# Optimization experiments

Hardware: AMD Instinct MI355X
Metric: run time of the kernel (lower is better)

## Reference

```python
import jax, jax.numpy as jnp
import numpy as np

B, S, D = 4, 2048, 1024
P = 2
N_FEAT = 16          # n_feature_know
N_REST = 16          # n_restore_know
R = 128              # knowledge_rank
D_SPACE = 64


def setup_inputs() -> dict:
    key = jax.random.key(0)
    ks = jax.random.split(key, 6)
    x = jax.random.normal(ks[0], (B, S, D), dtype=jnp.float32)
    # per-token routing weights for each of P feature paths, in [0,1)
    feature_paths = jax.random.uniform(ks[1], (P, B, S, N_FEAT), dtype=jnp.float32)
    f_know = jax.random.normal(ks[2], (N_FEAT, D, R), dtype=jnp.float32) * 0.02
    r_know = jax.random.normal(ks[3], (N_REST, R, D), dtype=jnp.float32) * 0.02
    feature_emb = jax.random.normal(ks[4], (N_FEAT, D_SPACE), dtype=jnp.float32)
    W_router = jax.random.normal(ks[5], (D_SPACE + R, N_REST), dtype=jnp.float32) * 0.05
    return {"x": x, "feature_paths": feature_paths, "f_know": f_know,
            "r_know": r_know, "feature_emb": feature_emb, "W_router": W_router}


def reference(x, feature_paths, f_know, r_know, feature_emb, W_router):
    # Feature projection into all N low-rank banks: [B,S,N,R]
    all_h = jnp.einsum('bsd,ndr->bsnr', x, f_know)
    # Weighted sum over banks per path: [P,B,S,R]
    h_all = jnp.einsum('bsnr,pbsn->pbsr', all_h, feature_paths)
    # Context for restore routing: [P,B,S,D_SPACE]
    neuron_ctx = jnp.einsum('pbsn,nd->pbsd', feature_paths, feature_emb)
    # restore_input = cat([neuron_ctx, h]) -> router -> softmax restore weights
    restore_input = jnp.concatenate([neuron_ctx, h_all], axis=-1)  # [P,B,S,D_SPACE+R]
    logits = jnp.einsum('pbsc,cn->pbsn', restore_input, W_router)
    w = jax.nn.softmax(logits, axis=-1)                            # [P,B,S,N_REST]
    # Restore + per-token weighted combine, summed over P paths: [B,S,D]
    output = jnp.einsum('pbsr,nrd,pbsn->bsd', h_all, r_know, w)
    restore_aux_loss = jnp.float32(0.0)
    return output, restore_aux_loss
```

## Files before the change

### kernel.cpp

```cpp
#include <hip/hip_runtime.h>

typedef __attribute__((ext_vector_type(16))) float f32x16;
typedef __bf16 bf16x8 __attribute__((ext_vector_type(8)));
typedef unsigned short ushort_t;

#define T_TOK 8192
#define DIM   1024
#define NRCOL 2048

#define VMW(n)  asm volatile("s_waitcnt vmcnt(" #n ")" ::: "memory")
#define SB0()   __builtin_amdgcn_sched_barrier(0)
#define BAR()   __builtin_amdgcn_s_barrier()

static __device__ __forceinline__ unsigned short f2bf(float f) {
  unsigned int u = __builtin_bit_cast(unsigned int, f);
  u += 0x7fffu + ((u >> 16) & 1u);
  return (unsigned short)(u >> 16);
}
static __device__ __forceinline__ float bfbits2f(unsigned int lo16) {
  return __builtin_bit_cast(float, lo16 << 16);
}
static __device__ __forceinline__ void gload16(const void* g, void* l) {
  __builtin_amdgcn_global_load_lds((const __attribute__((address_space(1))) void*)g,
                                   (__attribute__((address_space(3))) void*)l, 16, 0, 0);
}

__global__ __launch_bounds__(256) void cvt_f32_bf16(const float* __restrict__ in,
                                                    unsigned short* __restrict__ out,
                                                    int n4) {
  int i = blockIdx.x * 256 + threadIdx.x;
  const int stride = gridDim.x * 256;
  const float4* in4 = (const float4*)in;
  uint2* o4 = (uint2*)out;
  for (; i < n4; i += stride) {
    float4 v = in4[i];
    uint2 o;
    o.x = (unsigned)f2bf(v.x) | ((unsigned)f2bf(v.y) << 16);
    o.y = (unsigned)f2bf(v.z) | ((unsigned)f2bf(v.w) << 16);
    o4[i] = o;
  }
}

__global__ __launch_bounds__(256) void tcvt(const float* __restrict__ src,
                                            unsigned short* __restrict__ dst,
                                            int rows, int cols,
                                            long sstride, long dstride) {
  src += (size_t)blockIdx.z * sstride;
  dst += (size_t)blockIdx.z * dstride;
  __shared__ float tile[32][33];
  const int tx = threadIdx.x & 31, ty = threadIdx.x >> 5;
  const int r0 = blockIdx.y * 32, c0 = blockIdx.x * 32;
  #pragma unroll
  for (int i = 0; i < 32; i += 8)
    tile[ty + i][tx] = src[(size_t)(r0 + ty + i) * cols + c0 + tx];
  __syncthreads();
  #pragma unroll
  for (int i = 0; i < 32; i += 8)
    dst[(size_t)(c0 + ty + i) * rows + r0 + tx] = f2bf(tile[tx][ty + i]);
}

template<int K, bool OUT_BF16>
__global__ __launch_bounds__(512, 2) void gemm32(const ushort_t* __restrict__ A,
                                                 const ushort_t* __restrict__ Bt,
                                                 void* __restrict__ Cp, int N) {
  constexpr int nt = K / 64;
  __shared__ ushort_t As[3][128 * 64];
  __shared__ ushort_t Bs[3][256 * 64];

  const int tid = threadIdx.x;
  const int nx = gridDim.x;
  const int orig = blockIdx.y * nx + blockIdx.x;
  const int q = (nx * gridDim.y) >> 3;
  const int swz = (orig & 7) * q + (orig >> 3);
  const int bx = swz % nx, by = swz / nx;

  const int lane = tid & 63, wv = tid >> 6;
  const int wm = wv >> 2, wn = wv & 3;
  const int l31 = lane & 31, hi = lane >> 5;

  const ushort_t* Ab = A + (size_t)by * 128 * K;
  const ushort_t* Bb = Bt + (size_t)bx * 256 * K;

  const int srow = tid >> 3;
  const int sch = (tid & 7) ^ (srow & 7);
  const ushort_t* pA[2];
  const ushort_t* pB[4];
  #pragma unroll
  for (int r = 0; r < 2; ++r) pA[r] = Ab + (size_t)(r * 64 + srow) * K + sch * 8;
  #pragma unroll
  for (int r = 0; r < 4; ++r) pB[r] = Bb + (size_t)(r * 64 + srow) * K + sch * 8;
  const int dL = tid * 8;

  auto stage = [&](int s, int adv) {
    #pragma unroll
    for (int r = 0; r < 2; ++r) gload16(pA[r] + adv, (void*)&As[s][r * 4096 + dL]);
    #pragma unroll
    for (int r = 0; r < 4; ++r) gload16(pB[r] + adv, (void*)&Bs[s][r * 4096 + dL]);
  };

  int oA[2], oB[2];
  #pragma unroll
  for (int m = 0; m < 2; ++m) {
    const int r = wm * 64 + m * 32 + l31;
    oA[m] = r * 64 + (hi ^ (r & 7)) * 8;
  }
  #pragma unroll
  for (int n = 0; n < 2; ++n) {
    const int r = wn * 64 + n * 32 + l31;
    oB[n] = r * 64 + (hi ^ (r & 7)) * 8;
  }

  f32x16 acc[2][2];
  #pragma unroll
  for (int m = 0; m < 2; ++m)
    #pragma unroll
    for (int n = 0; n < 2; ++n)
      #pragma unroll
      for (int j = 0; j < 16; ++j) acc[m][n][j] = 0.f;

  stage(0, 0);
  stage(1, 64);
  VMW(6); SB0(); BAR(); SB0();

  #pragma unroll
  for (int t = 0; t < nt; ++t) {
    const int s = t % 3, s2 = (t + 2) % 3;
    bf16x8 av[2][4], bv[2][4];
    #pragma unroll
    for (int m = 0; m < 2; ++m)
      #pragma unroll
      for (int ks = 0; ks < 4; ++ks)
        av[m][ks] = *(const bf16x8*)&As[s][oA[m] ^ (ks * 16)];
    #pragma unroll
    for (int n = 0; n < 2; ++n)
      #pragma unroll
      for (int ks = 0; ks < 4; ++ks)
        bv[n][ks] = *(const bf16x8*)&Bs[s][oB[n] ^ (ks * 16)];
    if (t + 2 < nt) stage(s2, (t + 2) * 64);
    __builtin_amdgcn_s_setprio(1);
    #pragma unroll
    for (int ks = 0; ks < 4; ++ks)
      #pragma unroll
      for (int m = 0; m < 2; ++m)
        #pragma unroll
        for (int n = 0; n < 2; ++n)
          acc[m][n] = __builtin_amdgcn_mfma_f32_32x32x16_bf16(av[m][ks], bv[n][ks], acc[m][n], 0, 0, 0);
    __builtin_amdgcn_s_setprio(0);
    SB0();
    if (t + 2 < nt) { VMW(6); } else { VMW(0); }
    SB0(); BAR(); SB0();
  }

  #pragma unroll
  for (int m = 0; m < 2; ++m) {
    const int row0 = by * 128 + wm * 64 + m * 32 + 4 * hi;
    #pragma unroll
    for (int n = 0; n < 2; ++n) {
      const int col = bx * 256 + wn * 64 + n * 32 + l31;
      #pragma unroll
      for (int j = 0; j < 16; ++j) {
        const int grow = row0 + (j & 3) + 8 * (j >> 2);
        const size_t idx = (size_t)grow * N + col;
        if constexpr (OUT_BF16) ((ushort_t*)Cp)[idx] = f2bf(acc[m][n][j]);
        else                    ((float*)Cp)[idx] = acc[m][n][j];
      }
    }
  }
}

__global__ __launch_bounds__(256) void middle_kernel(const unsigned short* __restrict__ AH,
                                                     const float* __restrict__ fp,
                                                     const float* __restrict__ femb,
                                                     const float* __restrict__ Wr,
                                                     unsigned short* __restrict__ Mout,
                                                     float* __restrict__ auxout) {
  __shared__ float G[16][16];
  __shared__ float hs[4][2][128];
  __shared__ float wsm[4][2][16];
  const int tid = threadIdx.x;
  {
    const int n = tid >> 4, j = tid & 15;
    float s = 0.f;
    #pragma unroll
    for (int ds = 0; ds < 64; ++ds) s += femb[n * 64 + ds] * Wr[ds * 16 + j];
    G[n][j] = s;
  }
  const int wv = tid >> 6, l = tid & 63;
  const int t = blockIdx.x * 4 + wv;

  float p0[16], p1[16];
  #pragma unroll
  for (int n = 0; n < 16; ++n) {
    p0[n] = fp[t * 16 + n];
    p1[n] = fp[T_TOK * 16 + t * 16 + n];
  }

  float h00 = 0.f, h01 = 0.f, h10 = 0.f, h11 = 0.f;
  const unsigned short* ahrow = AH + (size_t)t * NRCOL;
  #pragma unroll
  for (int n = 0; n < 16; ++n) {
    const unsigned int v = *(const unsigned int*)(ahrow + n * 128 + 2 * l);
    const float a0 = bfbits2f(v & 0xffffu);
    const float a1 = bfbits2f(v >> 16);
    h00 += a0 * p0[n]; h01 += a1 * p0[n];
    h10 += a0 * p1[n]; h11 += a1 * p1[n];
  }
  hs[wv][0][2 * l] = h00; hs[wv][0][2 * l + 1] = h01;
  hs[wv][1][2 * l] = h10; hs[wv][1][2 * l + 1] = h11;
  __syncthreads();

  if (l < 32) {
    const int p = l >> 4, j = l & 15;
    float s = 0.f;
    #pragma unroll
    for (int n = 0; n < 16; ++n) s += (p ? p1[n] : p0[n]) * G[n][j];
    const float* hp = hs[wv][p];
    const float* wr = Wr + 64 * 16 + j;
    float s0 = 0.f, s1 = 0.f, s2 = 0.f, s3 = 0.f;
    #pragma unroll
    for (int r = 0; r < 128; r += 4) {
      s0 += hp[r]     * wr[(r)     * 16];
      s1 += hp[r + 1] * wr[(r + 1) * 16];
      s2 += hp[r + 2] * wr[(r + 2) * 16];
      s3 += hp[r + 3] * wr[(r + 3) * 16];
    }
    s += (s0 + s1) + (s2 + s3);
    float mx = s;
    #pragma unroll
    for (int d = 1; d < 16; d <<= 1) mx = fmaxf(mx, __shfl_xor(mx, d, 64));
    const float e = __expf(s - mx);
    float sum = e;
    #pragma unroll
    for (int d = 1; d < 16; d <<= 1) sum += __shfl_xor(sum, d, 64);
    wsm[wv][p][j] = e / sum;
  }
  __syncthreads();

  unsigned short* mrow = Mout + (size_t)t * NRCOL;
  #pragma unroll
  for (int n = 0; n < 16; ++n) {
    const float w0 = wsm[wv][0][n], w1 = wsm[wv][1][n];
    const float m0 = w0 * h00 + w1 * h10;
    const float m1 = w0 * h01 + w1 * h11;
    const unsigned int pk = (unsigned)f2bf(m0) | ((unsigned)f2bf(m1) << 16);
    *(unsigned int*)(mrow + n * 128 + 2 * l) = pk;
  }
  if (blockIdx.x == 0 && tid == 0) auxout[0] = 0.f;
}

extern "C" void kernel_launch(void* const* d_in, const int* in_sizes, int n_in,
                              void* d_out, int out_size, void* d_ws, size_t ws_size,
                              hipStream_t stream) {
  const float* x    = (const float*)d_in[0];
  const float* fp   = (const float*)d_in[1];
  const float* fk   = (const float*)d_in[2];
  const float* rk   = (const float*)d_in[3];
  const float* femb = (const float*)d_in[4];
  const float* Wr   = (const float*)d_in[5];
  float* out = (float*)d_out;

  char* ws = (char*)d_ws;
  unsigned short* Xbf = (unsigned short*)ws;
  unsigned short* W1t = (unsigned short*)(ws + 16u * 1024 * 1024);
  unsigned short* Mb  = (unsigned short*)ws;
  unsigned short* W2t = (unsigned short*)(ws + 32u * 1024 * 1024);
  unsigned short* AH  = (unsigned short*)(ws + 36u * 1024 * 1024);

  cvt_f32_bf16<<<2048, 256, 0, stream>>>(x, Xbf, (T_TOK * DIM) / 4);
  tcvt<<<dim3(128 / 32, 1024 / 32, 16), 256, 0, stream>>>(fk, W1t, 1024, 128,
                                                          1024L * 128, 128L * 1024);
  tcvt<<<dim3(1024 / 32, 2048 / 32, 1), 256, 0, stream>>>(rk, W2t, 2048, 1024, 0, 0);
  gemm32<1024, true><<<dim3(NRCOL / 256, T_TOK / 128), 512, 0, stream>>>(Xbf, W1t, AH, NRCOL);
  middle_kernel<<<T_TOK / 4, 256, 0, stream>>>(AH, fp, femb, Wr, Mb, out + 8388608);
  gemm32<2048, false><<<dim3(DIM / 256, T_TOK / 128), 512, 0, stream>>>(Mb, W2t, out, DIM);
}
```

Measured before the change: 126.4 us.

## Merge prep conversions into one kernel and retile GEMMs to 4-wave 16x16 MFMA

Folds the three conversion and transpose launches into a single prep kernel that dispatches on block index, removing launch overhead. Replaces the 512-thread 32x32x16 MFMA GEMM with a 256-thread template that uses 16x16x32 MFMA and larger per-wave tiles (256x128 for the first GEMM, 128x256 for the second). LDS fragment loads now happen per k-substep after the prefetch is issued. The per-wave accumulator footprint grows and occupancy is pinned to one block per CU, which may reduce latency hiding.

```diff
diff --git a/kernel.cpp b/kernel.cpp
--- a/kernel.cpp
+++ b/kernel.cpp
@@ -1,6 +1,6 @@
 #include <hip/hip_runtime.h>
 
-typedef __attribute__((ext_vector_type(16))) float f32x16;
+typedef __attribute__((ext_vector_type(4))) float f32x4;
 typedef __bf16 bf16x8 __attribute__((ext_vector_type(8)));
 typedef unsigned short ushort_t;
 
@@ -25,31 +25,45 @@
                                    (__attribute__((address_space(3))) void*)l, 16, 0, 0);
 }
 
-__global__ __launch_bounds__(256) void cvt_f32_bf16(const float* __restrict__ in,
-                                                    unsigned short* __restrict__ out,
-                                                    int n4) {
-  int i = blockIdx.x * 256 + threadIdx.x;
-  const int stride = gridDim.x * 256;
-  const float4* in4 = (const float4*)in;
-  uint2* o4 = (uint2*)out;
-  for (; i < n4; i += stride) {
-    float4 v = in4[i];
-    uint2 o;
-    o.x = (unsigned)f2bf(v.x) | ((unsigned)f2bf(v.y) << 16);
-    o.y = (unsigned)f2bf(v.z) | ((unsigned)f2bf(v.w) << 16);
-    o4[i] = o;
-  }
-}
-
-__global__ __launch_bounds__(256) void tcvt(const float* __restrict__ src,
-                                            unsigned short* __restrict__ dst,
-                                            int rows, int cols,
-                                            long sstride, long dstride) {
-  src += (size_t)blockIdx.z * sstride;
-  dst += (size_t)blockIdx.z * dstride;
+__global__ __launch_bounds__(256) void prep_kernel(const float* __restrict__ x,
+                                                   const float* __restrict__ fk,
+                                                   const float* __restrict__ rk,
+                                                   unsigned short* __restrict__ Xbf,
+                                                   unsigned short* __restrict__ W1t,
+                                                   unsigned short* __restrict__ W2t) {
+  const int bid = blockIdx.x, tid = threadIdx.x;
+  if (bid < 2048) {
+    const float4* in4 = (const float4*)x;
+    uint2* o4 = (uint2*)Xbf;
+    #pragma unroll
+    for (int it = 0; it < 4; ++it) {
+      const int i = bid * 256 + tid + it * 524288;
+      float4 v = in4[i];
+      uint2 o;
+      o.x = (unsigned)f2bf(v.x) | ((unsigned)f2bf(v.y) << 16);
+      o.y = (unsigned)f2bf(v.z) | ((unsigned)f2bf(v.w) << 16);
+      o4[i] = o;
+    }
+    return;
+  }
   __shared__ float tile[32][33];
-  const int tx = threadIdx.x & 31, ty = threadIdx.x >> 5;
-  const int r0 = blockIdx.y * 32, c0 = blockIdx.x * 32;
+  const float* src;
+  unsigned short* dst;
+  int rows, cols, r0, c0;
+  if (bid < 4096) {
+    const int b = bid - 2048;
+    const int z = b >> 7, rem = b & 127;
+    src = fk + (size_t)z * 1024 * 128;
+    dst = W1t + (size_t)z * 128 * 1024;
+    rows = 1024; cols = 128;
+    c0 = (rem & 3) * 32; r0 = (rem >> 2) * 32;
+  } else {
+    const int b = bid - 4096;
+    src = rk; dst = W2t;
+    rows = 2048; cols = 1024;
+    c0 = (b & 31) * 32; r0 = (b >> 5) * 32;
+  }
+  const int tx = tid & 31, ty = tid >> 5;
   #pragma unroll
   for (int i = 0; i < 32; i += 8)
     tile[ty + i][tx] = src[(size_t)(r0 + ty + i) * cols + c0 + tx];
@@ -59,13 +73,17 @@
     dst[(size_t)(c0 + ty + i) * rows + r0 + tx] = f2bf(tile[tx][ty + i]);
 }
 
-template<int K, bool OUT_BF16>
-__global__ __launch_bounds__(512, 2) void gemm32(const ushort_t* __restrict__ A,
-                                                 const ushort_t* __restrict__ Bt,
-                                                 void* __restrict__ Cp, int N) {
+template<int BM, int BN, int K, bool OUT_BF16>
+__global__ __launch_bounds__(256, 1) void gemmW(const ushort_t* __restrict__ A,
+                                                const ushort_t* __restrict__ Bt,
+                                                void* __restrict__ Cp, int N) {
   constexpr int nt = K / 64;
-  __shared__ ushort_t As[3][128 * 64];
-  __shared__ ushort_t Bs[3][256 * 64];
+  constexpr int MF = BM / 32;
+  constexpr int NF = BN / 32;
+  constexpr int AR = BM / 32;
+  constexpr int BR = BN / 32;
+  __shared__ ushort_t As[3][BM * 64];
+  __shared__ ushort_t Bs[3][BN * 64];
 
   const int tid = threadIdx.x;
   const int nx = gridDim.x;
@@ -75,92 +93,85 @@
   const int bx = swz % nx, by = swz / nx;
 
   const int lane = tid & 63, wv = tid >> 6;
-  const int wm = wv >> 2, wn = wv & 3;
-  const int l31 = lane & 31, hi = lane >> 5;
-
-  const ushort_t* Ab = A + (size_t)by * 128 * K;
-  const ushort_t* Bb = Bt + (size_t)bx * 256 * K;
+  const int wm = wv >> 1, wn = wv & 1;
+  const int lrow = lane & 15, lk = lane >> 4;
+
+  const ushort_t* Ab = A + (size_t)by * BM * K;
+  const ushort_t* Bb = Bt + (size_t)bx * BN * K;
 
   const int srow = tid >> 3;
   const int sch = (tid & 7) ^ (srow & 7);
-  const ushort_t* pA[2];
-  const ushort_t* pB[4];
-  #pragma unroll
-  for (int r = 0; r < 2; ++r) pA[r] = Ab + (size_t)(r * 64 + srow) * K + sch * 8;
-  #pragma unroll
-  for (int r = 0; r < 4; ++r) pB[r] = Bb + (size_t)(r * 64 + srow) * K + sch * 8;
+  const ushort_t* pA[AR];
+  const ushort_t* pB[BR];
+  #pragma unroll
+  for (int r = 0; r < AR; ++r) pA[r] = Ab + (size_t)(r * 32 + srow) * K + sch * 8;
+  #pragma unroll
+  for (int r = 0; r < BR; ++r) pB[r] = Bb + (size_t)(r * 32 + srow) * K + sch * 8;
   const int dL = tid * 8;
 
   auto stage = [&](int s, int adv) {
     #pragma unroll
-    for (int r = 0; r < 2; ++r) gload16(pA[r] + adv, (void*)&As[s][r * 4096 + dL]);
-    #pragma unroll
-    for (int r = 0; r < 4; ++r) gload16(pB[r] + adv, (void*)&Bs[s][r * 4096 + dL]);
+    for (int r = 0; r < AR; ++r) gload16(pA[r] + adv, (void*)&As[s][r * 2048 + dL]);
+    #pragma unroll
+    for (int r = 0; r < BR; ++r) gload16(pB[r] + adv, (void*)&Bs[s][r * 2048 + dL]);
   };
 
-  int oA[2], oB[2];
-  #pragma unroll
-  for (int m = 0; m < 2; ++m) {
-    const int r = wm * 64 + m * 32 + l31;
-    oA[m] = r * 64 + (hi ^ (r & 7)) * 8;
-  }
-  #pragma unroll
-  for (int n = 0; n < 2; ++n) {
-    const int r = wn * 64 + n * 32 + l31;
-    oB[n] = r * 64 + (hi ^ (r & 7)) * 8;
-  }
-
-  f32x16 acc[2][2];
-  #pragma unroll
-  for (int m = 0; m < 2; ++m)
-    #pragma unroll
-    for (int n = 0; n < 2; ++n)
-      #pragma unroll
-      for (int j = 0; j < 16; ++j) acc[m][n][j] = 0.f;
+  int oA[MF], oB[NF];
+  #pragma unroll
+  for (int m = 0; m < MF; ++m) {
+    const int r = wm * (BM / 2) + m * 16 + lrow;
+    oA[m] = r * 64 + (lk ^ (r & 7)) * 8;
+  }
+  #pragma unroll
+  for (int n = 0; n < NF; ++n) {
+    const int r = wn * (BN / 2) + n * 16 + lrow;
+    oB[n] = r * 64 + (lk ^ (r & 7)) * 8;
+  }
+
+  f32x4 acc[MF][NF];
+  #pragma unroll
+  for (int m = 0; m < MF; ++m)
+    #pragma unroll
+    for (int n = 0; n < NF; ++n)
+      acc[m][n] = (f32x4){0.f, 0.f, 0.f, 0.f};
 
   stage(0, 0);
   stage(1, 64);
-  VMW(6); SB0(); BAR(); SB0();
+  VMW(12); SB0(); BAR(); SB0();
 
   #pragma unroll
   for (int t = 0; t < nt; ++t) {
     const int s = t % 3, s2 = (t + 2) % 3;
-    bf16x8 av[2][4], bv[2][4];
-    #pragma unroll
-    for (int m = 0; m < 2; ++m)
-      #pragma unroll
-      for (int ks = 0; ks < 4; ++ks)
-        av[m][ks] = *(const bf16x8*)&As[s][oA[m] ^ (ks * 16)];
-    #pragma unroll
-    for (int n = 0; n < 2; ++n)
-      #pragma unroll
-      for (int ks = 0; ks < 4; ++ks)
-        bv[n][ks] = *(const bf16x8*)&Bs[s][oB[n] ^ (ks * 16)];
     if (t + 2 < nt) stage(s2, (t + 2) * 64);
-    __builtin_amdgcn_s_setprio(1);
-    #pragma unroll
-    for (int ks = 0; ks < 4; ++ks)
-      #pragma unroll
-      for (int m = 0; m < 2; ++m)
+    #pragma unroll
+    for (int ks = 0; ks < 2; ++ks) {
+      bf16x8 av[MF], bv[NF];
+      #pragma unroll
+      for (int m = 0; m < MF; ++m) av[m] = *(const bf16x8*)&As[s][oA[m] ^ (ks * 32)];
+      #pragma unroll
+      for (int n = 0; n < NF; ++n) bv[n] = *(const bf16x8*)&Bs[s][oB[n] ^ (ks * 32)];
+      __builtin_amdgcn_s_setprio(1);
+      #pragma unroll
+      for (int m = 0; m < MF; ++m)
         #pragma unroll
-        for (int n = 0; n < 2; ++n)
-          acc[m][n] = __builtin_amdgcn_mfma_f32_32x32x16_bf16(av[m][ks], bv[n][ks], acc[m][n], 0, 0, 0);
-    __builtin_amdgcn_s_setprio(0);
+        for (int n = 0; n < NF; ++n)
+          acc[m][n] = __builtin_amdgcn_mfma_f32_16x16x32_bf16(av[m], bv[n], acc[m][n], 0, 0, 0);
+      __builtin_amdgcn_s_setprio(0);
+    }
     SB0();
-    if (t + 2 < nt) { VMW(6); } else { VMW(0); }
+    if (t + 2 < nt) { VMW(12); } else { VMW(0); }
     SB0(); BAR(); SB0();
   }
 
   #pragma unroll
-  for (int m = 0; m < 2; ++m) {
-    const int row0 = by * 128 + wm * 64 + m * 32 + 4 * hi;
-    #pragma unroll
-    for (int n = 0; n < 2; ++n) {
-      const int col = bx * 256 + wn * 64 + n * 32 + l31;
-      #pragma unroll
-      for (int j = 0; j < 16; ++j) {
-        const int grow = row0 + (j & 3) + 8 * (j >> 2);
-        const size_t idx = (size_t)grow * N + col;
+  for (int m = 0; m < MF; ++m) {
+    const int row0 = by * BM + wm * (BM / 2) + m * 16 + lk * 4;
+    #pragma unroll
+    for (int n = 0; n < NF; ++n) {
+      const int col = bx * BN + wn * (BN / 2) + n * 16 + lrow;
+      #pragma unroll
+      for (int j = 0; j < 4; ++j) {
+        const size_t idx = (size_t)(row0 + j) * N + col;
         if constexpr (OUT_BF16) ((ushort_t*)Cp)[idx] = f2bf(acc[m][n][j]);
         else                    ((float*)Cp)[idx] = acc[m][n][j];
       }
@@ -266,11 +277,8 @@
   unsigned short* W2t = (unsigned short*)(ws + 32u * 1024 * 1024);
   unsigned short* AH  = (unsigned short*)(ws + 36u * 1024 * 1024);
 
-  cvt_f32_bf16<<<2048, 256, 0, stream>>>(x, Xbf, (T_TOK * DIM) / 4);
-  tcvt<<<dim3(128 / 32, 1024 / 32, 16), 256, 0, stream>>>(fk, W1t, 1024, 128,
-                                                          1024L * 128, 128L * 1024);
-  tcvt<<<dim3(1024 / 32, 2048 / 32, 1), 256, 0, stream>>>(rk, W2t, 2048, 1024, 0, 0);
-  gemm32<1024, true><<<dim3(NRCOL / 256, T_TOK / 128), 512, 0, stream>>>(Xbf, W1t, AH, NRCOL);
+  prep_kernel<<<6144, 256, 0, stream>>>(x, fk, rk, Xbf, W1t, W2t);
+  gemmW<256, 128, 1024, true><<<dim3(NRCOL / 128, T_TOK / 256), 256, 0, stream>>>(Xbf, W1t, AH, NRCOL);
   middle_kernel<<<T_TOK / 4, 256, 0, stream>>>(AH, fp, femb, Wr, Mb, out + 8388608);
-  gemm32<2048, false><<<dim3(DIM / 256, T_TOK / 128), 512, 0, stream>>>(Mb, W2t, out, DIM);
-}
+  gemmW<128, 256, 2048, false><<<dim3(DIM / 256, T_TOK / 128), 256, 0, stream>>>(Mb, W2t, out, DIM);
+}
```

Result: no change. 127.2 us (+0.7%).
